# Kernel optimization log

Hardware: AMD Instinct MI355X
Metric: run time of the kernel (lower is better)

## Reference

```python
import jax, jax.numpy as jnp
import numpy as np

N = 50000   # nodes
R = 4       # relation groups
E = 800000  # nnz per relation adjacency
ED = 200000 # decoded edges
H = 128     # hidden_dim
L = 64      # latent_dim
DH = 64     # decoder_hidden_dim


def setup_inputs() -> dict:
    key = jax.random.key(0)
    ks = iter(jax.random.split(key, 64))
    def nrm(shape, scale=1.0):
        return jax.random.normal(next(ks), shape, dtype=jnp.float32) * scale
    inp = {}
    inp["x_process"] = nrm((N, 62))
    inp["x_file"] = nrm((N, 37))
    inp["x_network"] = nrm((N, 37))
    def lin(prefix, din, dout):
        s = 1.0 / np.sqrt(din)
        inp[prefix + "_Ws"] = nrm((dout, din), s)
        inp[prefix + "_bs"] = nrm((dout,), s)
        inp[prefix + "_Wr"] = nrm((R, dout, din), s)
        inp[prefix + "_br"] = nrm((R, dout), s)
    lin("p1", 62, H); lin("p2", H, L)
    lin("f1", 37, H); lin("f2", H, L)
    lin("n1", 37, H); lin("n2", H, L)
    inp["gate_W"] = nrm((3, L), 1.0 / np.sqrt(L))
    inp["gate_b"] = nrm((3,), 0.1)
    inp["dec_W1"] = nrm((DH, 4 * L), 1.0 / np.sqrt(4 * L))
    inp["dec_b1"] = nrm((DH,), 0.1)
    inp["dec_W2"] = nrm((1, DH), 1.0 / np.sqrt(DH))
    inp["dec_b2"] = nrm((1,), 0.1)
    inp["adj_rows"] = jax.random.randint(next(ks), (R, E), 0, N, dtype=jnp.int32)
    inp["adj_cols"] = jax.random.randint(next(ks), (R, E), 0, N, dtype=jnp.int32)
    inp["adj_vals"] = jax.random.uniform(next(ks), (R, E), dtype=jnp.float32) * 0.1
    inp["edge_src"] = jax.random.randint(next(ks), (ED,), 0, N, dtype=jnp.int32)
    inp["edge_dst"] = jax.random.randint(next(ks), (ED,), 0, N, dtype=jnp.int32)
    return inp


def reference(x_process, x_file, x_network,
              p1_Ws, p1_bs, p1_Wr, p1_br, p2_Ws, p2_bs, p2_Wr, p2_br,
              f1_Ws, f1_bs, f1_Wr, f1_br, f2_Ws, f2_bs, f2_Wr, f2_br,
              n1_Ws, n1_bs, n1_Wr, n1_br, n2_Ws, n2_bs, n2_Wr, n2_br,
              gate_W, gate_b, dec_W1, dec_b1, dec_W2, dec_b2,
              adj_rows, adj_cols, adj_vals, edge_src, edge_dst):
    def spmm(rows, cols, vals, x):  # A @ x, A in COO: out[row] += val * x[col]
        return jax.ops.segment_sum(vals[:, None] * x[cols], rows, num_segments=N)

    def rgcn_layer(x, Ws, bs, Wr, br):
        out = x @ Ws.T + bs  # self_linear
        for r in range(R):
            out = out + spmm(adj_rows[r], adj_cols[r], adj_vals[r], x) @ Wr[r].T + br[r]
        return out / float(R + 1)

    def encoder(x, W1s, b1s, W1r, b1r, W2s, b2s, W2r, b2r):
        h = jax.nn.relu(rgcn_layer(x, W1s, b1s, W1r, b1r))
        # dropout p=0.0 / eval mode -> identity
        return rgcn_layer(h, W2s, b2s, W2r, b2r)

    z_p = encoder(x_process, p1_Ws, p1_bs, p1_Wr, p1_br, p2_Ws, p2_bs, p2_Wr, p2_br)
    z_f = encoder(x_file, f1_Ws, f1_bs, f1_Wr, f1_br, f2_Ws, f2_bs, f2_Wr, f2_br)
    z_n = encoder(x_network, n1_Ws, n1_bs, n1_Wr, n1_br, n2_Ws, n2_bs, n2_Wr, n2_br)

    # gated multi-view fusion: three Linear(latent,1) gates -> softmax over views
    scores = jnp.stack([z_p @ gate_W[0] + gate_b[0],
                        z_f @ gate_W[1] + gate_b[1],
                        z_n @ gate_W[2] + gate_b[2]], axis=1)  # [N, 3]
    alpha = jax.nn.softmax(scores, axis=1)
    z = alpha[:, 0:1] * z_p + alpha[:, 1:2] * z_f + alpha[:, 2:3] * z_n  # [N, L]

    # mlp edge decoder
    zs = z[edge_src]
    zd = z[edge_dst]
    feats = jnp.concatenate([zs, zd, zs * zd, jnp.abs(zs - zd)], axis=1)  # [ED, 4L]
    hid = jax.nn.relu(feats @ dec_W1.T + dec_b1)
    logits = (hid @ dec_W2.T + dec_b2)[:, 0]  # [ED]
    return logits
```

## Files before the change

kernel.cpp:

```cpp
#include <hip/hip_runtime.h>

#define N_NODES 50000
#define R_REL   4
#define E_NNZ   800000
#define ED_EDGES 200000
#define H_DIM   128
#define L_DIM   64

#define RN_TOTAL (R_REL * N_NODES)
#define ETOT     (R_REL * E_NNZ)

#define EPB   8192
#define NB    391
#define RBK   196
#define KBK   (R_REL * RBK)
#define HTOT  (KBK * NB)
#define SCB   300
#define MAXB  6144

#define WS_RP    0u
#define WS_HIST  800256u
#define WS_BSUM  2026496u
#define WS_CV    2030592u
#define WS_TMP   27630720u
#define WS_XALL  53230720u
#define WS_SP    72430720u
#define WS_SF    122030720u
#define WS_SN    151630720u
#define WS_HPR   181230720u
#define WS_HN    WS_TMP
#define WS_HF    WS_SP
#define WS_YSP   WS_XALL
#define WS_YSF   (WS_SP + 25600000u)
#define WS_YRP   WS_SF
#define WS_YRF   WS_SN
#define WS_YSN   WS_HPR
#define WS_YRN   WS_HF
#define WS_Z     194030720u

__device__ __forceinline__ ushort f2bf(float f) {
    unsigned u = __float_as_uint(f);
    unsigned r = (u + 0x7fffu + ((u >> 16) & 1u)) >> 16;
    return (ushort)r;
}
__device__ __forceinline__ float bf2f(ushort u) {
    return __uint_as_float(((unsigned)u) << 16);
}

__global__ void cast_xall_kernel(const float* __restrict__ xp, const float* __restrict__ xf,
                                 const float* __restrict__ xn, ushort* __restrict__ xall) {
    int i = blockIdx.x * 256 + threadIdx.x;
    if (i >= N_NODES * 192) return;
    int node = i / 192, k = i - node * 192;
    float v = 0.f;
    if (k < 62) v = xp[node * 62 + k];
    else if (k >= 64 && k < 138) {
        int j = k - 64, d = j >> 1;
        v = (j & 1) ? xn[node * 37 + d] : xf[node * 37 + d];
    }
    xall[i] = f2bf(v);
}

__global__ void radix_hist_kernel(const int* __restrict__ rows, int* __restrict__ H) {
    __shared__ int hist[KBK];
    int blk = blockIdx.x, t = threadIdx.x;
    for (int i = t; i < KBK; i += 256) hist[i] = 0;
    __syncthreads();
    int base = blk * EPB;
    #pragma unroll 1
    for (int i = 0; i < EPB / 256; i++) {
        int g = base + i * 256 + t;
        if (g < ETOT) {
            int r = g / E_NNZ;
            atomicAdd(&hist[r * RBK + (rows[g] >> 8)], 1);
        }
    }
    __syncthreads();
    for (int i = t; i < KBK; i += 256) H[i * NB + blk] = hist[i];
}

__global__ void scan_part_kernel(const int* __restrict__ H, int* __restrict__ bsum) {
    __shared__ int red[256];
    int base = blockIdx.x * 1024, t = threadIdx.x;
    int s = 0;
    #pragma unroll
    for (int i = 0; i < 4; i++) {
        int idx = base + i * 256 + t;
        if (idx < HTOT) s += H[idx];
    }
    red[t] = s; __syncthreads();
    for (int d = 128; d > 0; d >>= 1) {
        if (t < d) red[t] += red[t + d];
        __syncthreads();
    }
    if (t == 0) bsum[blockIdx.x] = red[0];
}

__global__ void scan_bsum_kernel(int* __restrict__ bsum, int* __restrict__ rp) {
    __shared__ int sh[512];
    int t = threadIdx.x;
    int v = (t < SCB) ? bsum[t] : 0;
    sh[t] = v; __syncthreads();
    for (int d = 1; d < 512; d <<= 1) {
        int u = (t >= d) ? sh[t - d] : 0;
        __syncthreads();
        sh[t] += u;
        __syncthreads();
    }
    if (t < SCB) bsum[t] = sh[t] - v;
    if (t == 0) rp[RN_TOTAL] = ETOT;
}

__global__ void scan_final_kernel(int* __restrict__ H, const int* __restrict__ bsum) {
    __shared__ int sh[256];
    int base = blockIdx.x * 1024, t = threadIdx.x;
    int c[4]; int s = 0;
    #pragma unroll
    for (int i = 0; i < 4; i++) {
        int idx = base + t * 4 + i;
        c[i] = (idx < HTOT) ? H[idx] : 0;
        s += c[i];
    }
    sh[t] = s; __syncthreads();
    for (int d = 1; d < 256; d <<= 1) {
        int u = (t >= d) ? sh[t - d] : 0;
        __syncthreads();
        sh[t] += u;
        __syncthreads();
    }
    int off = bsum[blockIdx.x] + sh[t] - s;
    #pragma unroll
    for (int i = 0; i < 4; i++) {
        int idx = base + t * 4 + i;
        if (idx < HTOT) H[idx] = off;
        off += c[i];
    }
}

__global__ void radix_scatter_kernel(const int* __restrict__ rows, const int* __restrict__ cols,
                                     const float* __restrict__ vals, const int* __restrict__ H,
                                     int2* __restrict__ tmp) {
    __shared__ int cur[KBK];
    int blk = blockIdx.x, t = threadIdx.x;
    for (int i = t; i < KBK; i += 256) cur[i] = H[i * NB + blk];
    __syncthreads();
    int base = blk * EPB;
    #pragma unroll 1
    for (int i = 0; i < EPB / 256; i++) {
        int g = base + i * 256 + t;
        if (g < ETOT) {
            int r = g / E_NNZ;
            int row = rows[g];
            int b = r * RBK + (row >> 8);
            int p = atomicAdd(&cur[b], 1);
            tmp[p] = make_int2(cols[g] | ((row & 255) << 16), __float_as_int(vals[g]));
        }
    }
}

__launch_bounds__(256)
__global__ void bucket_sort_kernel(const int2* __restrict__ tmp, const int* __restrict__ H,
                                   int* __restrict__ rp, int2* __restrict__ cse) {
    __shared__ int hist[256];
    __shared__ int sc[256];
    __shared__ int cur[256];
    __shared__ int2 eb[MAXB];
    int b = blockIdx.x, t = threadIdx.x;
    int start = H[b * NB];
    int end = (b == KBK - 1) ? ETOT : H[(b + 1) * NB];
    int cnt = end - start;
    bool useLds = (cnt <= MAXB);
    hist[t] = 0;
    __syncthreads();
    for (int i = t; i < cnt; i += 256) {
        int2 e = tmp[start + i];
        if (useLds) eb[i] = e;
        atomicAdd(&hist[(e.x >> 16) & 255], 1);
    }
    __syncthreads();
    sc[t] = hist[t]; __syncthreads();
    for (int d = 1; d < 256; d <<= 1) {
        int v = (t >= d) ? sc[t - d] : 0;
        __syncthreads();
        sc[t] += v;
        __syncthreads();
    }
    int pref = sc[t] - hist[t];
    int r = b / RBK, rh = b - r * RBK;
    int grow = rh * 256 + t;
    if (grow < N_NODES) rp[r * N_NODES + grow] = start + pref;
    cur[t] = start + pref;
    __syncthreads();
    for (int i = t; i < cnt; i += 256) {
        int2 e = useLds ? eb[i] : tmp[start + i];
        int rl = (e.x >> 16) & 255;
        int p = atomicAdd(&cur[rl], 1);
        cse[p] = make_int2(e.x & 0xFFFF, e.y);
    }
}

__global__ void spmm1_all_kernel(const ushort* __restrict__ xall,
                                 const int* __restrict__ rp, const int2* __restrict__ cse,
                                 float* __restrict__ Sp, float* __restrict__ Sf,
                                 float* __restrict__ Sn) {
    int wave = threadIdx.x >> 6, lane = threadIdx.x & 63;
    int row = blockIdx.x * 4 + wave;
    if (row >= N_NODES) return;
    bool lp = lane < 62, lf = lane < 37;
    int opx = lane;
    int ofn = 64 + 2 * lane;
    for (int r = 0; r < R_REL; r++) {
        int e0 = rp[r * N_NODES + row], e1 = rp[r * N_NODES + row + 1];
        float ap = 0.f, af = 0.f, an = 0.f;
        int e = e0;
        for (; e + 4 <= e1; e += 4) {
            int2 q0 = cse[e], q1 = cse[e + 1], q2 = cse[e + 2], q3 = cse[e + 3];
            const ushort* b0 = xall + (size_t)q0.x * 192;
            const ushort* b1 = xall + (size_t)q1.x * 192;
            const ushort* b2 = xall + (size_t)q2.x * 192;
            const ushort* b3 = xall + (size_t)q3.x * 192;
            ushort  p0 = b0[opx], p1 = b1[opx], p2 = b2[opx], p3 = b3[opx];
            ushort2 u0 = *(const ushort2*)&b0[ofn];
            ushort2 u1 = *(const ushort2*)&b1[ofn];
            ushort2 u2 = *(const ushort2*)&b2[ofn];
            ushort2 u3 = *(const ushort2*)&b3[ofn];
            float v0 = __int_as_float(q0.y), v1 = __int_as_float(q1.y);
            float v2 = __int_as_float(q2.y), v3 = __int_as_float(q3.y);
            ap += v0 * bf2f(p0) + v1 * bf2f(p1) + v2 * bf2f(p2) + v3 * bf2f(p3);
            af += v0 * bf2f(u0.x) + v1 * bf2f(u1.x) + v2 * bf2f(u2.x) + v3 * bf2f(u3.x);
            an += v0 * bf2f(u0.y) + v1 * bf2f(u1.y) + v2 * bf2f(u2.y) + v3 * bf2f(u3.y);
        }
        for (; e < e1; e++) {
            int2 q = cse[e];
            const ushort* b = xall + (size_t)q.x * 192;
            float v = __int_as_float(q.y);
            ap += v * bf2f(b[opx]);
            ushort2 u = *(const ushort2*)&b[ofn];
            af += v * bf2f(u.x);
            an += v * bf2f(u.y);
        }
        if (lp) Sp[row * 248 + r * 62 + lane] = ap;
        if (lf) { Sf[row * 148 + r * 37 + lane] = af; Sn[row * 148 + r * 37 + lane] = an; }
    }
}

__launch_bounds__(256)
__global__ void gemm1_kernel(const float* __restrict__ x, const float* __restrict__ S,
                             const float* __restrict__ Ws, const float* __restrict__ bs,
                             const float* __restrict__ Wr, const float* __restrict__ br,
                             float* __restrict__ h, int din) {
    __shared__ float sA[64 * 63];
    __shared__ float sW[62 * 132];
    int t = threadIdx.x;
    int i0 = blockIdx.x * 64;
    int rg = t >> 5, cg = t & 31;
    float acc[8][4] = {};
    for (int s = 0; s < 5; s++) {
        const float* Aptr; int astride;
        if (s == 0) { Aptr = x; astride = din; }
        else        { Aptr = S + (s - 1) * din; astride = 4 * din; }
        const float* Wp = (s == 0) ? Ws : (Wr + (s - 1) * H_DIM * din);
        __syncthreads();
        for (int idx = t; idx < 64 * din; idx += 256) {
            int rr = idx / din, k = idx - rr * din;
            int grow = i0 + rr;
            sA[rr * 63 + k] = (grow < N_NODES) ? Aptr[grow * astride + k] : 0.f;
        }
        for (int idx = t; idx < H_DIM * din; idx += 256) {
            int j = idx / din, k = idx - j * din;
            sW[k * 132 + j] = Wp[j * din + k];
        }
        __syncthreads();
        for (int k = 0; k < din; k++) {
            float a[8];
            #pragma unroll
            for (int rr = 0; rr < 8; rr++) a[rr] = sA[(rg * 8 + rr) * 63 + k];
            float4 w = *(const float4*)&sW[k * 132 + cg * 4];
            #pragma unroll
            for (int rr = 0; rr < 8; rr++) {
                acc[rr][0] += a[rr] * w.x; acc[rr][1] += a[rr] * w.y;
                acc[rr][2] += a[rr] * w.z; acc[rr][3] += a[rr] * w.w;
            }
        }
    }
    int j0 = cg * 4;
    float btot[4];
    #pragma unroll
    for (int cc = 0; cc < 4; cc++) {
        float b = bs[j0 + cc];
        #pragma unroll
        for (int r = 0; r < R_REL; r++) b += br[r * H_DIM + j0 + cc];
        btot[cc] = b;
    }
    #pragma unroll
    for (int rr = 0; rr < 8; rr++) {
        int grow = i0 + rg * 8 + rr;
        if (grow < N_NODES) {
            float4 o;
            o.x = fmaxf((acc[rr][0] + btot[0]) * 0.2f, 0.f);
            o.y = fmaxf((acc[rr][1] + btot[1]) * 0.2f, 0.f);
            o.z = fmaxf((acc[rr][2] + btot[2]) * 0.2f, 0.f);
            o.w = fmaxf((acc[rr][3] + btot[3]) * 0.2f, 0.f);
            *(float4*)&h[grow * H_DIM + j0] = o;
        }
    }
}

__launch_bounds__(256)
__global__ void gemm2_kernel(const float* __restrict__ h, const float* __restrict__ Ws2,
                             const float* __restrict__ Wr2, float* __restrict__ Yself,
                             ushort* __restrict__ Yrel) {
    __shared__ float sA[128 * 65];
    __shared__ float sW[64 * 68];
    int t = threadIdx.x;
    int i0 = blockIdx.x * 128;
    int ct = blockIdx.y;
    int rg = t >> 4, cg = t & 15;
    const float* Wp = (ct == 0) ? Ws2 : (Wr2 + (ct - 1) * 64 * H_DIM);
    float acc[8][4] = {};
    for (int kc = 0; kc < 2; kc++) {
        __syncthreads();
        for (int idx = t; idx < 128 * 64; idx += 256) {
            int rr = idx >> 6, k = idx & 63;
            int grow = i0 + rr;
            sA[rr * 65 + k] = (grow < N_NODES) ? h[grow * H_DIM + kc * 64 + k] : 0.f;
        }
        for (int idx = t; idx < 64 * 64; idx += 256) {
            int j = idx >> 6, k = idx & 63;
            sW[k * 68 + j] = Wp[j * H_DIM + kc * 64 + k];
        }
        __syncthreads();
        for (int k = 0; k < 64; k++) {
            float a[8];
            #pragma unroll
            for (int rr = 0; rr < 8; rr++) a[rr] = sA[(rg * 8 + rr) * 65 + k];
            float4 w = *(const float4*)&sW[k * 68 + cg * 4];
            #pragma unroll
            for (int rr = 0; rr < 8; rr++) {
                acc[rr][0] += a[rr] * w.x; acc[rr][1] += a[rr] * w.y;
                acc[rr][2] += a[rr] * w.z; acc[rr][3] += a[rr] * w.w;
            }
        }
    }
    #pragma unroll
    for (int rr = 0; rr < 8; rr++) {
        int grow = i0 + rg * 8 + rr;
        if (grow < N_NODES) {
            if (ct == 0) {
                float4 o = make_float4(acc[rr][0], acc[rr][1], acc[rr][2], acc[rr][3]);
                *(float4*)&Yself[(size_t)grow * 64 + cg * 4] = o;
            } else {
                ushort4 o;
                o.x = f2bf(acc[rr][0]); o.y = f2bf(acc[rr][1]);
                o.z = f2bf(acc[rr][2]); o.w = f2bf(acc[rr][3]);
                *(ushort4*)&Yrel[(size_t)grow * 256 + (ct - 1) * 64 + cg * 4] = o;
            }
        }
    }
}

__global__ void spmm2z_all_kernel(const float* __restrict__ Ysp, const ushort* __restrict__ Yrp,
                                  const float* __restrict__ Ysf, const ushort* __restrict__ Yrf,
                                  const float* __restrict__ Ysn, const ushort* __restrict__ Yrn,
                                  const int* __restrict__ rp, const int2* __restrict__ cse,
                                  const float* __restrict__ p_bs, const float* __restrict__ p_br,
                                  const float* __restrict__ f_bs, const float* __restrict__ f_br,
                                  const float* __restrict__ n_bs, const float* __restrict__ n_br,
                                  const float* __restrict__ gW, const float* __restrict__ gb,
                                  float* __restrict__ z) {
    int wave = threadIdx.x >> 6, lane = threadIdx.x & 63;
    int row = blockIdx.x * 4 + wave;
    if (row >= N_NODES) return;
    float aP = Ysp[(size_t)row * 64 + lane] + p_bs[lane]
             + p_br[lane] + p_br[64 + lane] + p_br[128 + lane] + p_br[192 + lane];
    float aF = Ysf[(size_t)row * 64 + lane] + f_bs[lane]
             + f_br[lane] + f_br[64 + lane] + f_br[128 + lane] + f_br[192 + lane];
    float aN = Ysn[(size_t)row * 64 + lane] + n_bs[lane]
             + n_br[lane] + n_br[64 + lane] + n_br[128 + lane] + n_br[192 + lane];
    for (int r = 0; r < R_REL; r++) {
        int e0 = rp[r * N_NODES + row], e1 = rp[r * N_NODES + row + 1];
        const ushort* yp = Yrp + r * 64 + lane;
        const ushort* yf = Yrf + r * 64 + lane;
        const ushort* yn = Yrn + r * 64 + lane;
        int e = e0;
        for (; e + 4 <= e1; e += 4) {
            int2 q0 = cse[e], q1 = cse[e + 1], q2 = cse[e + 2], q3 = cse[e + 3];
            size_t o0 = (size_t)q0.x * 256, o1 = (size_t)q1.x * 256;
            size_t o2 = (size_t)q2.x * 256, o3 = (size_t)q3.x * 256;
            float pp0 = bf2f(yp[o0]), pp1 = bf2f(yp[o1]), pp2 = bf2f(yp[o2]), pp3 = bf2f(yp[o3]);
            float ff0 = bf2f(yf[o0]), ff1 = bf2f(yf[o1]), ff2 = bf2f(yf[o2]), ff3 = bf2f(yf[o3]);
            float nn0 = bf2f(yn[o0]), nn1 = bf2f(yn[o1]), nn2 = bf2f(yn[o2]), nn3 = bf2f(yn[o3]);
            float v0 = __int_as_float(q0.y), v1 = __int_as_float(q1.y);
            float v2 = __int_as_float(q2.y), v3 = __int_as_float(q3.y);
            aP += v0 * pp0 + v1 * pp1 + v2 * pp2 + v3 * pp3;
            aF += v0 * ff0 + v1 * ff1 + v2 * ff2 + v3 * ff3;
            aN += v0 * nn0 + v1 * nn1 + v2 * nn2 + v3 * nn3;
        }
        for (; e < e1; e++) {
            int2 q = cse[e];
            size_t o = (size_t)q.x * 256;
            float v = __int_as_float(q.y);
            aP += v * bf2f(yp[o]);
            aF += v * bf2f(yf[o]);
            aN += v * bf2f(yn[o]);
        }
    }
    aP *= 0.2f; aF *= 0.2f; aN *= 0.2f;
    float sp = aP * gW[lane], sf = aF * gW[64 + lane], sn = aN * gW[128 + lane];
    #pragma unroll
    for (int d = 32; d >= 1; d >>= 1) {
        sp += __shfl_xor(sp, d);
        sf += __shfl_xor(sf, d);
        sn += __shfl_xor(sn, d);
    }
    sp += gb[0]; sf += gb[1]; sn += gb[2];
    float m = fmaxf(sp, fmaxf(sf, sn));
    float ep = __expf(sp - m), ef = __expf(sf - m), en = __expf(sn - m);
    float inv = 1.f / (ep + ef + en);
    z[row * 64 + lane] = (ep * aP + ef * aF + en * aN) * inv;
}

__launch_bounds__(256)
__global__ void decoder_kernel(const float* __restrict__ z, const int* __restrict__ esrc,
                               const int* __restrict__ edst, const float* __restrict__ w1,
                               const float* __restrict__ b1, const float* __restrict__ w2,
                               const float* __restrict__ b2, float* __restrict__ out) {
    int e = blockIdx.x * blockDim.x + threadIdx.x;
    if (e >= ED_EDGES) return;
    const float* zs = z + (size_t)esrc[e] * 64;
    const float* zd = z + (size_t)edst[e] * 64;
    float hid[64];
    #pragma unroll
    for (int j = 0; j < 64; j++) hid[j] = b1[j];
    #pragma unroll 1
    for (int kc = 0; kc < 64; kc += 8) {
        float a[8], b[8], p[8], q[8];
        #pragma unroll
        for (int kk = 0; kk < 8; kk++) {
            a[kk] = zs[kc + kk]; b[kk] = zd[kc + kk];
            p[kk] = a[kk] * b[kk]; q[kk] = fabsf(a[kk] - b[kk]);
        }
        #pragma unroll
        for (int j = 0; j < 64; j++) {
            const float* wrow = w1 + j * 256 + kc;
            float s = hid[j];
            #pragma unroll
            for (int kk = 0; kk < 8; kk++) {
                s += a[kk] * wrow[kk] + b[kk] * wrow[64 + kk]
                   + p[kk] * wrow[128 + kk] + q[kk] * wrow[192 + kk];
            }
            hid[j] = s;
        }
    }
    float logit = b2[0];
    #pragma unroll
    for (int j = 0; j < 64; j++) logit += fmaxf(hid[j], 0.f) * w2[j];
    out[e] = logit;
}

extern "C" void kernel_launch(void* const* d_in, const int* in_sizes, int n_in,
                              void* d_out, int out_size, void* d_ws, size_t ws_size,
                              hipStream_t stream) {
    const float* x_p = (const float*)d_in[0];
    const float* x_f = (const float*)d_in[1];
    const float* x_n = (const float*)d_in[2];
    const float* p1_Ws = (const float*)d_in[3];  const float* p1_bs = (const float*)d_in[4];
    const float* p1_Wr = (const float*)d_in[5];  const float* p1_br = (const float*)d_in[6];
    const float* p2_Ws = (const float*)d_in[7];  const float* p2_bs = (const float*)d_in[8];
    const float* p2_Wr = (const float*)d_in[9];  const float* p2_br = (const float*)d_in[10];
    const float* f1_Ws = (const float*)d_in[11]; const float* f1_bs = (const float*)d_in[12];
    const float* f1_Wr = (const float*)d_in[13]; const float* f1_br = (const float*)d_in[14];
    const float* f2_Ws = (const float*)d_in[15]; const float* f2_bs = (const float*)d_in[16];
    const float* f2_Wr = (const float*)d_in[17]; const float* f2_br = (const float*)d_in[18];
    const float* n1_Ws = (const float*)d_in[19]; const float* n1_bs = (const float*)d_in[20];
    const float* n1_Wr = (const float*)d_in[21]; const float* n1_br = (const float*)d_in[22];
    const float* n2_Ws = (const float*)d_in[23]; const float* n2_bs = (const float*)d_in[24];
    const float* n2_Wr = (const float*)d_in[25]; const float* n2_br = (const float*)d_in[26];
    const float* gate_W = (const float*)d_in[27]; const float* gate_b = (const float*)d_in[28];
    const float* dec_W1 = (const float*)d_in[29]; const float* dec_b1 = (const float*)d_in[30];
    const float* dec_W2 = (const float*)d_in[31]; const float* dec_b2 = (const float*)d_in[32];
    const int*   adj_rows = (const int*)d_in[33];
    const int*   adj_cols = (const int*)d_in[34];
    const float* adj_vals = (const float*)d_in[35];
    const int*   edge_src = (const int*)d_in[36];
    const int*   edge_dst = (const int*)d_in[37];

    char* ws = (char*)d_ws;
    int*    rp   = (int*)(ws + WS_RP);
    int*    H    = (int*)(ws + WS_HIST);
    int*    bsum = (int*)(ws + WS_BSUM);
    int2*   cse  = (int2*)(ws + WS_CV);
    int2*   tmp  = (int2*)(ws + WS_TMP);
    ushort* xall = (ushort*)(ws + WS_XALL);
    float*  S_p = (float*)(ws + WS_SP);
    float*  S_f = (float*)(ws + WS_SF);
    float*  S_n = (float*)(ws + WS_SN);
    float*  h_p = (float*)(ws + WS_HPR);
    float*  h_f = (float*)(ws + WS_HF);
    float*  h_n = (float*)(ws + WS_HN);
    float*  Ys_p = (float*)(ws + WS_YSP);  ushort* Yr_p = (ushort*)(ws + WS_YRP);
    float*  Ys_f = (float*)(ws + WS_YSF);  ushort* Yr_f = (ushort*)(ws + WS_YRF);
    float*  Ys_n = (float*)(ws + WS_YSN);  ushort* Yr_n = (ushort*)(ws + WS_YRN);
    float*  z   = (float*)(ws + WS_Z);
    float*  out = (float*)d_out;

    cast_xall_kernel<<<(N_NODES * 192 + 255) / 256, 256, 0, stream>>>(x_p, x_f, x_n, xall);

    radix_hist_kernel<<<NB, 256, 0, stream>>>(adj_rows, H);
    scan_part_kernel<<<SCB, 256, 0, stream>>>(H, bsum);
    scan_bsum_kernel<<<1, 512, 0, stream>>>(bsum, rp);
    scan_final_kernel<<<SCB, 256, 0, stream>>>(H, bsum);
    radix_scatter_kernel<<<NB, 256, 0, stream>>>(adj_rows, adj_cols, adj_vals, H, tmp);
    bucket_sort_kernel<<<KBK, 256, 0, stream>>>(tmp, H, rp, cse);

    spmm1_all_kernel<<<N_NODES / 4, 256, 0, stream>>>(xall, rp, cse, S_p, S_f, S_n);

    int g1 = (N_NODES + 63) / 64;
    gemm1_kernel<<<g1, 256, 0, stream>>>(x_p, S_p, p1_Ws, p1_bs, p1_Wr, p1_br, h_p, 62);
    gemm1_kernel<<<g1, 256, 0, stream>>>(x_f, S_f, f1_Ws, f1_bs, f1_Wr, f1_br, h_f, 37);
    gemm1_kernel<<<g1, 256, 0, stream>>>(x_n, S_n, n1_Ws, n1_bs, n1_Wr, n1_br, h_n, 37);

    dim3 g2((N_NODES + 127) / 128, 5);
    gemm2_kernel<<<g2, 256, 0, stream>>>(h_p, p2_Ws, p2_Wr, Ys_p, Yr_p);
    gemm2_kernel<<<g2, 256, 0, stream>>>(h_f, f2_Ws, f2_Wr, Ys_f, Yr_f);
    gemm2_kernel<<<g2, 256, 0, stream>>>(h_n, n2_Ws, n2_Wr, Ys_n, Yr_n);

    spmm2z_all_kernel<<<N_NODES / 4, 256, 0, stream>>>(
        Ys_p, Yr_p, Ys_f, Yr_f, Ys_n, Yr_n, rp, cse,
        p2_bs, p2_br, f2_bs, f2_br, n2_bs, n2_br, gate_W, gate_b, z);

    decoder_kernel<<<(ED_EDGES + 255) / 256, 256, 0, stream>>>(
        z, edge_src, edge_dst, dec_W1, dec_b1, dec_W2, dec_b2, out);
}
```

Before: 1.429 ms.

## Precompute per-node decoder projections and map one wave per edge

```diff
diff --git a/kernel.cpp b/kernel.cpp
--- a/kernel.cpp
+++ b/kernel.cpp
@@ -37,6 +37,8 @@
 #define WS_YSN   WS_HPR
 #define WS_YRN   WS_HF
 #define WS_Z     194030720u
+#define WS_ZA    WS_SP
+#define WS_ZB    (WS_SP + 12800000u)
 
 __device__ __forceinline__ ushort f2bf(float f) {
     unsigned u = __float_as_uint(f);
@@ -421,41 +423,80 @@
 }
 
 __launch_bounds__(256)
-__global__ void decoder_kernel(const float* __restrict__ z, const int* __restrict__ esrc,
-                               const int* __restrict__ edst, const float* __restrict__ w1,
-                               const float* __restrict__ b1, const float* __restrict__ w2,
-                               const float* __restrict__ b2, float* __restrict__ out) {
-    int e = blockIdx.x * blockDim.x + threadIdx.x;
-    if (e >= ED_EDGES) return;
-    const float* zs = z + (size_t)esrc[e] * 64;
-    const float* zd = z + (size_t)edst[e] * 64;
-    float hid[64];
-    #pragma unroll
-    for (int j = 0; j < 64; j++) hid[j] = b1[j];
-    #pragma unroll 1
-    for (int kc = 0; kc < 64; kc += 8) {
-        float a[8], b[8], p[8], q[8];
+__global__ void dec_prep_kernel(const float* __restrict__ z, const float* __restrict__ w1,
+                                const float* __restrict__ b1, float* __restrict__ za,
+                                float* __restrict__ zb, int nwaves) {
+    int lane = threadIdx.x & 63;
+    int wid = (blockIdx.x * blockDim.x + threadIdx.x) >> 6;
+    float wa[64], wb[64];
+    const float* wr = w1 + lane * 256;
+    #pragma unroll
+    for (int k = 0; k < 64; k += 4) {
+        float4 c = *(const float4*)&wr[k];
+        wa[k] = c.x; wa[k + 1] = c.y; wa[k + 2] = c.z; wa[k + 3] = c.w;
+        float4 d = *(const float4*)&wr[64 + k];
+        wb[k] = d.x; wb[k + 1] = d.y; wb[k + 2] = d.z; wb[k + 3] = d.w;
+    }
+    float b1v = b1[lane];
+    for (int n = wid; n < N_NODES; n += nwaves) {
+        const float4* zp = (const float4*)(z + (size_t)n * 64);
+        float ha = b1v, hb = 0.f;
         #pragma unroll
-        for (int kk = 0; kk < 8; kk++) {
-            a[kk] = zs[kc + kk]; b[kk] = zd[kc + kk];
-            p[kk] = a[kk] * b[kk]; q[kk] = fabsf(a[kk] - b[kk]);
-        }
+        for (int kc = 0; kc < 16; kc++) {
+            float4 v = zp[kc];
+            int k = kc * 4;
+            ha += v.x * wa[k] + v.y * wa[k + 1] + v.z * wa[k + 2] + v.w * wa[k + 3];
+            hb += v.x * wb[k] + v.y * wb[k + 1] + v.z * wb[k + 2] + v.w * wb[k + 3];
+        }
+        za[(size_t)n * 64 + lane] = ha;
+        zb[(size_t)n * 64 + lane] = hb;
+    }
+}
+
+__launch_bounds__(256)
+__global__ void decoder2_kernel(const float* __restrict__ z, const float* __restrict__ za,
+                                const float* __restrict__ zb, const int* __restrict__ esrc,
+                                const int* __restrict__ edst, const float* __restrict__ w1,
+                                const float* __restrict__ w2, const float* __restrict__ b2,
+                                float* __restrict__ out, int nwaves) {
+    int lane = threadIdx.x & 63;
+    int wid = (blockIdx.x * blockDim.x + threadIdx.x) >> 6;
+    float wc[64], wd[64];
+    const float* wr = w1 + lane * 256;
+    #pragma unroll
+    for (int k = 0; k < 64; k += 4) {
+        float4 c = *(const float4*)&wr[128 + k];
+        wc[k] = c.x; wc[k + 1] = c.y; wc[k + 2] = c.z; wc[k + 3] = c.w;
+        float4 d = *(const float4*)&wr[192 + k];
+        wd[k] = d.x; wd[k + 1] = d.y; wd[k + 2] = d.z; wd[k + 3] = d.w;
+    }
+    float w2j = w2[lane];
+    float b2v = b2[0];
+    for (int e = wid; e < ED_EDGES; e += nwaves) {
+        int s = esrc[e];
+        int d = edst[e];
+        const float4* zsp = (const float4*)(z + (size_t)s * 64);
+        const float4* zdp = (const float4*)(z + (size_t)d * 64);
+        float hid = za[(size_t)s * 64 + lane] + zb[(size_t)d * 64 + lane];
         #pragma unroll
-        for (int j = 0; j < 64; j++) {
-            const float* wrow = w1 + j * 256 + kc;
-            float s = hid[j];
-            #pragma unroll
-            for (int kk = 0; kk < 8; kk++) {
-                s += a[kk] * wrow[kk] + b[kk] * wrow[64 + kk]
-                   + p[kk] * wrow[128 + kk] + q[kk] * wrow[192 + kk];
-            }
-            hid[j] = s;
-        }
-    }
-    float logit = b2[0];
-    #pragma unroll
-    for (int j = 0; j < 64; j++) logit += fmaxf(hid[j], 0.f) * w2[j];
-    out[e] = logit;
+        for (int kc = 0; kc < 16; kc++) {
+            float4 a = zsp[kc];
+            float4 b = zdp[kc];
+            int k = kc * 4;
+            float p0 = a.x * b.x, q0 = fabsf(a.x - b.x);
+            float p1 = a.y * b.y, q1 = fabsf(a.y - b.y);
+            float p2 = a.z * b.z, q2 = fabsf(a.z - b.z);
+            float p3 = a.w * b.w, q3 = fabsf(a.w - b.w);
+            hid += p0 * wc[k] + q0 * wd[k]
+                 + p1 * wc[k + 1] + q1 * wd[k + 1]
+                 + p2 * wc[k + 2] + q2 * wd[k + 2]
+                 + p3 * wc[k + 3] + q3 * wd[k + 3];
+        }
+        float v = fmaxf(hid, 0.f) * w2j;
+        #pragma unroll
+        for (int m = 32; m >= 1; m >>= 1) v += __shfl_xor(v, m);
+        if (lane == 0) out[e] = v + b2v;
+    }
 }
 
 extern "C" void kernel_launch(void* const* d_in, const int* in_sizes, int n_in,
@@ -502,6 +543,8 @@
     float*  Ys_f = (float*)(ws + WS_YSF);  ushort* Yr_f = (ushort*)(ws + WS_YRF);
     float*  Ys_n = (float*)(ws + WS_YSN);  ushort* Yr_n = (ushort*)(ws + WS_YRN);
     float*  z   = (float*)(ws + WS_Z);
+    float*  za  = (float*)(ws + WS_ZA);
+    float*  zb  = (float*)(ws + WS_ZB);
     float*  out = (float*)d_out;
 
     cast_xall_kernel<<<(N_NODES * 192 + 255) / 256, 256, 0, stream>>>(x_p, x_f, x_n, xall);
@@ -529,6 +572,7 @@
         Ys_p, Yr_p, Ys_f, Yr_f, Ys_n, Yr_n, rp, cse,
         p2_bs, p2_br, f2_bs, f2_br, n2_bs, n2_br, gate_W, gate_b, z);
 
-    decoder_kernel<<<(ED_EDGES + 255) / 256, 256, 0, stream>>>(
-        z, edge_src, edge_dst, dec_W1, dec_b1, dec_W2, dec_b2, out);
-}
+    dec_prep_kernel<<<256, 256, 0, stream>>>(z, dec_W1, dec_b1, za, zb, 256 * 4);
+    decoder2_kernel<<<1024, 256, 0, stream>>>(
+        z, za, zb, edge_src, edge_dst, dec_W1, dec_W2, dec_b2, out, 1024 * 4);
+}
```

Measured after the change: 1.637 ms. +14.6%, slower.
